# Performance work log

Hardware: AMD Instinct MI355X
Metric: run time of the kernel (lower is better)

## Reference

```python
import jax, jax.numpy as jnp
import numpy as np

NEGATIVE_RATIO = 3.0


def setup_inputs() -> dict:
    key = jax.random.key(0)
    k1, k2, k3, k4, k5 = jax.random.split(key, 5)
    B, N, C = 64, 8732, 81  # batch, num_priors (SSD300), num_classes (COCO)
    pred_conf = jax.random.normal(k1, (B, N, C), dtype=jnp.float32)
    pred_loc = jax.random.normal(k2, (B, N, 4), dtype=jnp.float32)
    labels = jax.random.randint(k3, (B, N), 1, C)
    is_pos = jax.random.uniform(k4, (B, N)) < 0.03
    labels = jnp.where(is_pos, labels, 0)
    labels = labels.at[:, 0].set(1)  # guarantee >=1 positive per image
    gt_conf = jax.nn.one_hot(labels, C, dtype=jnp.float32)
    pos = (labels > 0)[..., None].astype(jnp.float32)
    gt_loc = jax.random.normal(k5, (B, N, 4), dtype=jnp.float32) * pos
    return {"pred_conf": pred_conf, "pred_loc": pred_loc,
            "gt_conf": gt_conf, "gt_loc": gt_loc}


def reference(pred_conf, pred_loc, gt_conf, gt_loc):
    B, N, _ = pred_conf.shape
    # ----- conf loss: cross entropy against one-hot gt -----
    conf_loss = -(jax.nn.log_softmax(pred_conf, axis=-1) * gt_conf).sum(-1)  # [B, N]
    pos_mask = gt_conf[:, :, 0] == 0  # non-background priors
    num_pos = pos_mask.sum(-1).astype(pred_conf.dtype)  # [B]
    pos_conf_loss = jnp.where(pos_mask, conf_loss, 0.0).sum(-1)  # [B]
    # ----- hard negative mining: keep losses strictly above k-th largest negative loss -----
    num_neg = num_pos * NEGATIVE_RATIO  # [B], float
    neg_loss = jnp.where(pos_mask, 0.0, conf_loss)  # zero out positives
    sorted_desc = -jnp.sort(-neg_loss, axis=-1)  # descending per row
    k = jnp.clip(num_neg.astype(jnp.int32), 0, N - 1)  # [B]
    thresh = jnp.take_along_axis(sorted_desc, k[:, None], axis=-1)  # [B, 1]
    neg_mask = neg_loss > thresh  # only true on negatives (pos entries are 0)
    neg_conf_loss = jnp.where(neg_mask, conf_loss, 0.0).sum(-1)  # [B]
    conf_total = pos_conf_loss / num_pos + neg_conf_loss / num_neg  # [B]
    # ----- loc loss: smooth L1 on priors with nonzero gt_loc -----
    loc_mask = gt_loc != 0  # [B, N, 4]
    num_pos_loc = jnp.any(loc_mask, axis=-1).sum(-1).astype(pred_loc.dtype)  # [B]
    diff = jnp.abs(pred_loc - gt_loc)
    smooth_l1 = jnp.where(diff < 1.0, 0.5 * diff * diff, diff - 0.5)
    loc_total = jnp.where(loc_mask, smooth_l1, 0.0).sum((-1, -2)) / num_pos_loc  # [B]
    return (conf_total + loc_total).mean()
```

## Files before the change

### kernel.cpp

```cpp
#include <hip/hip_runtime.h>
#include <math.h>

#define BB 64
#define NN 8732
#define CC 81
#define ROWS 64
#define CBX ((NN + ROWS - 1) / ROWS)
#define LBX 5

__global__ void init_kernel(unsigned* acc, float* out) {
    int i = threadIdx.x;
    if (i < 4 * BB) acc[i] = 0u;
    if (i == 0) out[0] = 0.f;
}

__global__ __launch_bounds__(256) void fused_kernel(
        const float* __restrict__ pred_conf,
        const float* __restrict__ gt_conf,
        const float* __restrict__ pred_loc,
        const float* __restrict__ gt_loc,
        float* __restrict__ neg_loss,
        int* __restrict__ num_pos,
        float* __restrict__ pos_sum,
        float* __restrict__ loc_cnt,
        float* __restrict__ loc_sum) {
    const int b   = blockIdx.y;
    const int tid = threadIdx.x;

    if (blockIdx.x >= CBX) {
        const int lb = blockIdx.x - CBX;
        const float4* pl = (const float4*)pred_loc;
        const float4* gl = (const float4*)gt_loc;
        float sum = 0.f, cnt = 0.f;
        #pragma unroll
        for (int j = 0; j < 8; ++j) {
            int n = lb * 2048 + j * 256 + tid;
            if (n < NN) {
                size_t idx = (size_t)b * NN + n;
                float4 p = pl[idx];
                float4 g = gl[idx];
                bool any = false;
                float pv[4] = {p.x, p.y, p.z, p.w};
                float gv[4] = {g.x, g.y, g.z, g.w};
                #pragma unroll
                for (int c = 0; c < 4; ++c) {
                    if (gv[c] != 0.f) {
                        any = true;
                        float d = fabsf(pv[c] - gv[c]);
                        sum += (d < 1.f) ? 0.5f * d * d : d - 0.5f;
                    }
                }
                if (any) cnt += 1.f;
            }
        }
        for (int o = 32; o; o >>= 1) {
            sum += __shfl_down(sum, o, 64);
            cnt += __shfl_down(cnt, o, 64);
        }
        __shared__ float ls_sum, ls_cnt;
        if (tid == 0) { ls_sum = 0.f; ls_cnt = 0.f; }
        __syncthreads();
        if ((tid & 63) == 0) { atomicAdd(&ls_sum, sum); atomicAdd(&ls_cnt, cnt); }
        __syncthreads();
        if (tid == 0) { atomicAdd(&loc_sum[b], ls_sum); atomicAdd(&loc_cnt[b], ls_cnt); }
        return;
    }

    __shared__ float lbuf[ROWS * CC + 8];
    __shared__ int   s_cnt;
    __shared__ float s_sum;

    const int rowBase = blockIdx.x * ROWS;
    const int nrows   = min(ROWS, NN - rowBase);
    const size_t TOTF = (size_t)BB * NN * CC;

    if (tid == 0) { s_cnt = 0; s_sum = 0.f; }

    const size_t seg = ((size_t)b * NN + rowBase) * CC;
    const int    cnt = nrows * CC;
    const size_t a0  = seg & ~(size_t)3;
    const int  shift = (int)(seg - a0);
    const int   tot4 = (shift + cnt + 3) >> 2;

    const float4* g4 = (const float4*)(pred_conf + a0);
    float4*       l4 = (float4*)lbuf;
    for (int i = tid; i < tot4; i += 256) {
        size_t gf = a0 + 4 * (size_t)i;
        if (gf + 4 <= TOTF) {
            l4[i] = g4[i];
        } else {
            #pragma unroll
            for (int c = 0; c < 4; ++c)
                lbuf[4 * i + c] = (gf + c < TOTF) ? pred_conf[gf + c] : 0.f;
        }
    }
    __syncthreads();

    const int r = tid >> 2;
    const int h = tid & 3;
    if (r < nrows) {
        const int c0 = h * 20 + (h > 0 ? 1 : 0);
        const int nc = (h == 0) ? 21 : 20;
        const float* row = lbuf + shift + r * CC;
        const size_t gbase = ((size_t)b * NN + rowBase + r) * CC;
        const float gt0 = gt_conf[gbase];

        float v[21];
        #pragma unroll
        for (int j = 0; j < 21; ++j)
            v[j] = (j < nc) ? row[c0 + j] : -1e30f;

        float m = v[0];
        #pragma unroll
        for (int j = 1; j < 21; ++j) m = fmaxf(m, v[j]);
        m = fmaxf(m, __shfl_xor(m, 1, 64));
        m = fmaxf(m, __shfl_xor(m, 2, 64));

        float e = 0.f;
        #pragma unroll
        for (int j = 0; j < 21; ++j) e += __expf(v[j] - m);
        e += __shfl_xor(e, 1, 64);
        e += __shfl_xor(e, 2, 64);

        const bool pos = (gt0 == 0.f);
        float x_sel = v[0];
        if (pos) {
            float d = 0.f;
            #pragma unroll
            for (int j = 0; j < 21; ++j)
                if (j < nc) d += gt_conf[gbase + c0 + j] * v[j];
            d += __shfl_xor(d, 1, 64);
            d += __shfl_xor(d, 2, 64);
            x_sel = d;
        }

        const float loss = m + __logf(e) - x_sel;
        if (h == 0) {
            neg_loss[(size_t)b * NN + rowBase + r] = pos ? 0.f : loss;
            if (pos) { atomicAdd(&s_cnt, 1); atomicAdd(&s_sum, loss); }
        }
    }
    __syncthreads();
    if (tid == 0 && s_cnt) {
        atomicAdd(&num_pos[b], s_cnt);
        atomicAdd(&pos_sum[b], s_sum);
    }
}

__global__ __launch_bounds__(256) void select_kernel(
        const float* __restrict__ neg_loss,
        const int*   __restrict__ num_pos,
        const float* __restrict__ pos_sum,
        const float* __restrict__ loc_cnt,
        const float* __restrict__ loc_sum,
        float* __restrict__ out) {
    const int b    = blockIdx.x;
    const int tid  = threadIdx.x;
    const int lane = tid & 63;
    __shared__ unsigned vals[NN];
    __shared__ unsigned hist[256];
    __shared__ unsigned sh_prefix, sh_r;
    __shared__ float    s_part[4];

    #pragma unroll 4
    for (int i = tid; i < NN; i += 256)
        vals[i] = __float_as_uint(neg_loss[(size_t)b * NN + i]);

    const int np = num_pos[b];
    const int k  = min(3 * np, NN - 1);
    if (tid == 0) { sh_prefix = 0u; sh_r = (unsigned)k; }
    __syncthreads();

    unsigned prefix_mask = 0u;
    for (int p = 3; p >= 0; --p) {
        const unsigned pref = sh_prefix;
        const unsigned r    = sh_r;
        hist[tid] = 0u;
        __syncthreads();

        for (int i0 = 0; i0 < NN; i0 += 256) {
            const int i = i0 + tid;
            const bool act = (i < NN) && ((vals[i] & prefix_mask) == pref);
            const unsigned v   = act ? vals[i] : 0u;
            const unsigned bin = (v >> (8 * p)) & 255u;
            unsigned long long mm = __ballot(act);
            #pragma unroll
            for (int bit = 0; bit < 8; ++bit) {
                unsigned long long s = __ballot(act && ((bin >> bit) & 1u));
                mm &= ((bin >> bit) & 1u) ? s : ~s;
            }
            if (act && ((mm & ((1ull << lane) - 1ull)) == 0ull))
                atomicAdd(&hist[bin], (unsigned)__popcll(mm));
        }
        __syncthreads();

        if (tid < 64) {
            const unsigned h0 = hist[4 * tid + 0];
            const unsigned h1 = hist[4 * tid + 1];
            const unsigned h2 = hist[4 * tid + 2];
            const unsigned h3 = hist[4 * tid + 3];
            unsigned T = h0 + h1 + h2 + h3;
            #pragma unroll
            for (int off = 1; off < 64; off <<= 1) {
                unsigned t2 = __shfl_down(T, off, 64);
                if (tid + off < 64) T += t2;
            }
            unsigned Tn = __shfl_down(T, 1, 64);
            if (tid == 63) Tn = 0u;
            const unsigned S4 = Tn, S3 = S4 + h3, S2 = S3 + h2, S1 = S2 + h1, S0 = S1 + h0;
            int bin = -1; unsigned Slo = 0u;
            if      (S1 <= r && r < S0) { bin = 4 * tid + 0; Slo = S1; }
            else if (S2 <= r && r < S1) { bin = 4 * tid + 1; Slo = S2; }
            else if (S3 <= r && r < S2) { bin = 4 * tid + 2; Slo = S3; }
            else if (S4 <= r && r < S3) { bin = 4 * tid + 3; Slo = S4; }
            if (bin >= 0) {
                sh_r = r - Slo;
                sh_prefix = pref | ((unsigned)bin << (8 * p));
            }
        }
        __syncthreads();
        prefix_mask |= 0xFFu << (8 * p);
    }

    const float thresh = __uint_as_float(sh_prefix);
    float s = 0.f;
    #pragma unroll 4
    for (int i = tid; i < NN; i += 256) {
        float v = __uint_as_float(vals[i]);
        if (v > thresh) s += v;
    }
    for (int o = 32; o; o >>= 1) s += __shfl_down(s, o, 64);
    if (lane == 0) s_part[tid >> 6] = s;
    __syncthreads();
    if (tid == 0) {
        float neg_sum = s_part[0] + s_part[1] + s_part[2] + s_part[3];
        float npf = (float)np;
        float res = pos_sum[b] / npf + neg_sum / (3.0f * npf) + loc_sum[b] / loc_cnt[b];
        atomicAdd(out, res * (1.0f / BB));
    }
}

extern "C" void kernel_launch(void* const* d_in, const int* in_sizes, int n_in,
                              void* d_out, int out_size, void* d_ws, size_t ws_size,
                              hipStream_t stream) {
    const float* pred_conf = (const float*)d_in[0];
    const float* pred_loc  = (const float*)d_in[1];
    const float* gt_conf   = (const float*)d_in[2];
    const float* gt_loc    = (const float*)d_in[3];

    float* neg      = (float*)d_ws;
    int*   num_pos  = (int*)(neg + (size_t)BB * NN);
    float* pos_sum  = (float*)(num_pos + BB);
    float* loc_cnt  = pos_sum + BB;
    float* loc_sum  = loc_cnt + BB;

    init_kernel<<<1, 256, 0, stream>>>((unsigned*)num_pos, (float*)d_out);

    dim3 fgrid(CBX + LBX, BB);
    fused_kernel<<<fgrid, 256, 0, stream>>>(pred_conf, gt_conf, pred_loc, gt_loc,
                                            neg, num_pos, pos_sum, loc_cnt, loc_sum);

    select_kernel<<<BB, 256, 0, stream>>>(neg, num_pos, pos_sum, loc_cnt, loc_sum,
                                          (float*)d_out);
}
```

Before: 425.1 us.

## Register-prefetch next conf tile while computing current tile, four tiles per block

Each conf block now processes four 64-row tiles in sequence. While it computes the softmax for the current tile out of LDS, it holds the next tile's pred_conf in registers loaded as float4, so global loads overlap with compute. This cuts the block count by four and raises register use (24 extra floats per thread), which may lower occupancy and reduce how much the hardware can overlap across blocks.

```diff
diff --git a/kernel.cpp b/kernel.cpp
--- a/kernel.cpp
+++ b/kernel.cpp
@@ -4,14 +4,23 @@
 #define BB 64
 #define NN 8732
 #define CC 81
-#define ROWS 64
-#define CBX ((NN + ROWS - 1) / ROWS)
+#define TR 64
+#define TPB 4
+#define CBX ((NN + TR * TPB - 1) / (TR * TPB))
 #define LBX 5
 
 __global__ void init_kernel(unsigned* acc, float* out) {
     int i = threadIdx.x;
     if (i < 4 * BB) acc[i] = 0u;
     if (i == 0) out[0] = 0.f;
+}
+
+__device__ __forceinline__ float4 ld4g(const float* __restrict__ p, size_t gf, size_t TOTF) {
+    if (gf + 4 <= TOTF) return *(const float4*)(p + gf);
+    float4 r; float* rp = (float*)&r;
+    #pragma unroll
+    for (int c = 0; c < 4; ++c) rp[c] = (gf + c < TOTF) ? p[gf + c] : 0.f;
+    return r;
 }
 
 __global__ __launch_bounds__(256) void fused_kernel(
@@ -66,80 +75,107 @@
         return;
     }
 
-    __shared__ float lbuf[ROWS * CC + 8];
+    __shared__ float lbuf[TR * CC + 8];
     __shared__ int   s_cnt;
     __shared__ float s_sum;
-
-    const int rowBase = blockIdx.x * ROWS;
-    const int nrows   = min(ROWS, NN - rowBase);
+    float4* l4 = (float4*)lbuf;
+
     const size_t TOTF = (size_t)BB * NN * CC;
-
-    if (tid == 0) { s_cnt = 0; s_sum = 0.f; }
-
-    const size_t seg = ((size_t)b * NN + rowBase) * CC;
-    const int    cnt = nrows * CC;
-    const size_t a0  = seg & ~(size_t)3;
-    const int  shift = (int)(seg - a0);
-    const int   tot4 = (shift + cnt + 3) >> 2;
-
-    const float4* g4 = (const float4*)(pred_conf + a0);
-    float4*       l4 = (float4*)lbuf;
-    for (int i = tid; i < tot4; i += 256) {
-        size_t gf = a0 + 4 * (size_t)i;
-        if (gf + 4 <= TOTF) {
-            l4[i] = g4[i];
-        } else {
-            #pragma unroll
-            for (int c = 0; c < 4; ++c)
-                lbuf[4 * i + c] = (gf + c < TOTF) ? pred_conf[gf + c] : 0.f;
-        }
-    }
-    __syncthreads();
-
+    const int tile0 = blockIdx.x * TPB;
     const int r = tid >> 2;
     const int h = tid & 3;
-    if (r < nrows) {
-        const int c0 = h * 20 + (h > 0 ? 1 : 0);
-        const int nc = (h == 0) ? 21 : 20;
-        const float* row = lbuf + shift + r * CC;
-        const size_t gbase = ((size_t)b * NN + rowBase + r) * CC;
-        const float gt0 = gt_conf[gbase];
-
-        float v[21];
+
+    if (tid == 0) { s_cnt = 0; s_sum = 0.f; }
+
+    float4 rv[6];
+    float  gt0p;
+    int rowBn = tile0 * TR;
+    int nrn   = min(TR, NN - rowBn);
+    size_t a0n; int shn, t4n;
+    {
+        size_t seg = ((size_t)b * NN + rowBn) * CC;
+        a0n = seg & ~(size_t)3; shn = (int)(seg - a0n);
+        t4n = (shn + nrn * CC + 3) >> 2;
+    }
+    #pragma unroll
+    for (int j = 0; j < 6; ++j) {
+        int i = tid + 256 * j;
+        if (i < t4n) rv[j] = ld4g(pred_conf, a0n + 4 * (size_t)i, TOTF);
+    }
+    gt0p = (r < nrn) ? gt_conf[((size_t)b * NN + rowBn + r) * CC] : 1.f;
+
+    for (int t = 0; t < TPB; ++t) {
+        const int   c_rowB = rowBn, c_nr = nrn, c_sh = shn, c_t4 = t4n;
+        const float c_gt0  = gt0p;
+        if (c_rowB >= NN) break;
+
+        __syncthreads();
         #pragma unroll
-        for (int j = 0; j < 21; ++j)
-            v[j] = (j < nc) ? row[c0 + j] : -1e30f;
-
-        float m = v[0];
-        #pragma unroll
-        for (int j = 1; j < 21; ++j) m = fmaxf(m, v[j]);
-        m = fmaxf(m, __shfl_xor(m, 1, 64));
-        m = fmaxf(m, __shfl_xor(m, 2, 64));
-
-        float e = 0.f;
-        #pragma unroll
-        for (int j = 0; j < 21; ++j) e += __expf(v[j] - m);
-        e += __shfl_xor(e, 1, 64);
-        e += __shfl_xor(e, 2, 64);
-
-        const bool pos = (gt0 == 0.f);
-        float x_sel = v[0];
-        if (pos) {
-            float d = 0.f;
+        for (int j = 0; j < 6; ++j) {
+            int i = tid + 256 * j;
+            if (i < c_t4) l4[i] = rv[j];
+        }
+
+        const int nrowB = (tile0 + t + 1) * TR;
+        if (t + 1 < TPB && nrowB < NN) {
+            rowBn = nrowB; nrn = min(TR, NN - nrowB);
+            size_t seg = ((size_t)b * NN + nrowB) * CC;
+            a0n = seg & ~(size_t)3; shn = (int)(seg - a0n);
+            t4n = (shn + nrn * CC + 3) >> 2;
+            #pragma unroll
+            for (int j = 0; j < 6; ++j) {
+                int i = tid + 256 * j;
+                if (i < t4n) rv[j] = ld4g(pred_conf, a0n + 4 * (size_t)i, TOTF);
+            }
+            gt0p = (r < nrn) ? gt_conf[((size_t)b * NN + rowBn + r) * CC] : 1.f;
+        } else {
+            rowBn = NN;
+        }
+        __syncthreads();
+
+        if (r < c_nr) {
+            const int c0 = h * 20 + (h > 0 ? 1 : 0);
+            const int nc = (h == 0) ? 21 : 20;
+            const float* row = lbuf + c_sh + r * CC;
+            const size_t gbase = ((size_t)b * NN + c_rowB + r) * CC;
+
+            float v[21];
             #pragma unroll
             for (int j = 0; j < 21; ++j)
-                if (j < nc) d += gt_conf[gbase + c0 + j] * v[j];
-            d += __shfl_xor(d, 1, 64);
-            d += __shfl_xor(d, 2, 64);
-            x_sel = d;
-        }
-
-        const float loss = m + __logf(e) - x_sel;
-        if (h == 0) {
-            neg_loss[(size_t)b * NN + rowBase + r] = pos ? 0.f : loss;
-            if (pos) { atomicAdd(&s_cnt, 1); atomicAdd(&s_sum, loss); }
-        }
-    }
+                v[j] = (j < nc) ? row[c0 + j] : -1e30f;
+
+            float m = v[0];
+            #pragma unroll
+            for (int j = 1; j < 21; ++j) m = fmaxf(m, v[j]);
+            m = fmaxf(m, __shfl_xor(m, 1, 64));
+            m = fmaxf(m, __shfl_xor(m, 2, 64));
+
+            float e = 0.f;
+            #pragma unroll
+            for (int j = 0; j < 21; ++j) e += __expf(v[j] - m);
+            e += __shfl_xor(e, 1, 64);
+            e += __shfl_xor(e, 2, 64);
+
+            const bool pos = (c_gt0 == 0.f);
+            float x_sel = v[0];
+            if (pos) {
+                float d = 0.f;
+                #pragma unroll
+                for (int j = 0; j < 21; ++j)
+                    if (j < nc) d += gt_conf[gbase + c0 + j] * v[j];
+                d += __shfl_xor(d, 1, 64);
+                d += __shfl_xor(d, 2, 64);
+                x_sel = d;
+            }
+
+            const float loss = m + __logf(e) - x_sel;
+            if (h == 0) {
+                neg_loss[(size_t)b * NN + c_rowB + r] = pos ? 0.f : loss;
+                if (pos) { atomicAdd(&s_cnt, 1); atomicAdd(&s_sum, loss); }
+            }
+        }
+    }
+
     __syncthreads();
     if (tid == 0 && s_cnt) {
         atomicAdd(&num_pos[b], s_cnt);
```

After: 415.9 us. 1.02x faster.

## Replace LDS-staged conf tiles with wave-strip register pipeline, 16 lanes per row

Applied to the files above, without the earlier changes.

Drops the shared-memory staging of 64-row pred_conf tiles and the block-wide syncs. Each wave now walks a strip of 32 priors four rows at a time, with 16 lanes per row, and software-prefetches the next group's logits into registers while computing the current group. The loc-loss path now issues per-wave global atomics instead of a shared-memory pre-reduction. The intent is to remove LDS round trips and barriers and to hide load latency. In exchange, global loads become strided per lane (less coalesced than float4 staging) and there are more global atomics.

```diff
diff --git a/kernel.cpp b/kernel.cpp
--- a/kernel.cpp
+++ b/kernel.cpp
@@ -4,8 +4,10 @@
 #define BB 64
 #define NN 8732
 #define CC 81
-#define ROWS 64
-#define CBX ((NN + ROWS - 1) / ROWS)
+#define STRIP 32
+#define GPW 8
+#define CWAVES ((NN + STRIP - 1) / STRIP)
+#define CBX ((CWAVES + 3) / 4)
 #define LBX 5
 
 __global__ void init_kernel(unsigned* acc, float* out) {
@@ -57,93 +59,126 @@
             sum += __shfl_down(sum, o, 64);
             cnt += __shfl_down(cnt, o, 64);
         }
-        __shared__ float ls_sum, ls_cnt;
-        if (tid == 0) { ls_sum = 0.f; ls_cnt = 0.f; }
-        __syncthreads();
-        if ((tid & 63) == 0) { atomicAdd(&ls_sum, sum); atomicAdd(&ls_cnt, cnt); }
-        __syncthreads();
-        if (tid == 0) { atomicAdd(&loc_sum[b], ls_sum); atomicAdd(&loc_cnt[b], ls_cnt); }
+        if ((tid & 63) == 0) {
+            atomicAdd(&loc_sum[b], sum);
+            atomicAdd(&loc_cnt[b], cnt);
+        }
         return;
     }
 
-    __shared__ float lbuf[ROWS * CC + 8];
-    __shared__ int   s_cnt;
-    __shared__ float s_sum;
-
-    const int rowBase = blockIdx.x * ROWS;
-    const int nrows   = min(ROWS, NN - rowBase);
-    const size_t TOTF = (size_t)BB * NN * CC;
-
-    if (tid == 0) { s_cnt = 0; s_sum = 0.f; }
-
-    const size_t seg = ((size_t)b * NN + rowBase) * CC;
-    const int    cnt = nrows * CC;
-    const size_t a0  = seg & ~(size_t)3;
-    const int  shift = (int)(seg - a0);
-    const int   tot4 = (shift + cnt + 3) >> 2;
-
-    const float4* g4 = (const float4*)(pred_conf + a0);
-    float4*       l4 = (float4*)lbuf;
-    for (int i = tid; i < tot4; i += 256) {
-        size_t gf = a0 + 4 * (size_t)i;
-        if (gf + 4 <= TOTF) {
-            l4[i] = g4[i];
-        } else {
-            #pragma unroll
-            for (int c = 0; c < 4; ++c)
-                lbuf[4 * i + c] = (gf + c < TOTF) ? pred_conf[gf + c] : 0.f;
-        }
-    }
-    __syncthreads();
-
-    const int r = tid >> 2;
-    const int h = tid & 3;
-    if (r < nrows) {
-        const int c0 = h * 20 + (h > 0 ? 1 : 0);
-        const int nc = (h == 0) ? 21 : 20;
-        const float* row = lbuf + shift + r * CC;
-        const size_t gbase = ((size_t)b * NN + rowBase + r) * CC;
-        const float gt0 = gt_conf[gbase];
-
-        float v[21];
-        #pragma unroll
-        for (int j = 0; j < 21; ++j)
-            v[j] = (j < nc) ? row[c0 + j] : -1e30f;
-
-        float m = v[0];
-        #pragma unroll
-        for (int j = 1; j < 21; ++j) m = fmaxf(m, v[j]);
-        m = fmaxf(m, __shfl_xor(m, 1, 64));
-        m = fmaxf(m, __shfl_xor(m, 2, 64));
-
-        float e = 0.f;
-        #pragma unroll
-        for (int j = 0; j < 21; ++j) e += __expf(v[j] - m);
-        e += __shfl_xor(e, 1, 64);
-        e += __shfl_xor(e, 2, 64);
-
-        const bool pos = (gt0 == 0.f);
-        float x_sel = v[0];
-        if (pos) {
-            float d = 0.f;
-            #pragma unroll
-            for (int j = 0; j < 21; ++j)
-                if (j < nc) d += gt_conf[gbase + c0 + j] * v[j];
-            d += __shfl_xor(d, 1, 64);
-            d += __shfl_xor(d, 2, 64);
-            x_sel = d;
-        }
-
-        const float loss = m + __logf(e) - x_sel;
-        if (h == 0) {
-            neg_loss[(size_t)b * NN + rowBase + r] = pos ? 0.f : loss;
-            if (pos) { atomicAdd(&s_cnt, 1); atomicAdd(&s_sum, loss); }
-        }
-    }
-    __syncthreads();
-    if (tid == 0 && s_cnt) {
-        atomicAdd(&num_pos[b], s_cnt);
-        atomicAdd(&pos_sum[b], s_sum);
+    const int wave = tid >> 6;
+    const int lane = tid & 63;
+    const int sub  = lane & 15;
+    const int rw   = lane >> 4;
+
+    const int wid   = blockIdx.x * 4 + wave;
+    const int strip = wid * STRIP;
+    int ng = 0;
+    if (strip < NN) {
+        int nst = NN - strip; if (nst > STRIP) nst = STRIP;
+        ng = (nst + 3) >> 2;
+    }
+
+    int   my_cnt = 0;
+    float my_sum = 0.f;
+
+    float cv0, cv1, cv2, cv3, cv4, cv5, cg0;
+    int   c_n = 0; bool c_valid = false;
+
+    if (ng > 0) {
+        int n = strip + rw;
+        c_valid = (n < NN);
+        c_n = n;
+        int ncl = c_valid ? n : (NN - 1);
+        size_t base = ((size_t)b * NN + ncl) * CC;
+        cv0 = pred_conf[base + sub +  0];
+        cv1 = pred_conf[base + sub + 16];
+        cv2 = pred_conf[base + sub + 32];
+        cv3 = pred_conf[base + sub + 48];
+        cv4 = pred_conf[base + sub + 64];
+        cv5 = (sub == 0) ? pred_conf[base + 80] : -1e30f;
+        cg0 = gt_conf[base];
+    }
+
+    #pragma unroll
+    for (int gi = 0; gi < GPW; ++gi) {
+        if (gi >= ng) break;
+
+        float nv0, nv1, nv2, nv3, nv4, nv5, ngt0;
+        int   n_n = 0; bool n_valid = false;
+        if (gi + 1 < ng) {
+            int n = strip + (gi + 1) * 4 + rw;
+            n_valid = (n < NN);
+            n_n = n;
+            int ncl = n_valid ? n : (NN - 1);
+            size_t base = ((size_t)b * NN + ncl) * CC;
+            nv0 = pred_conf[base + sub +  0];
+            nv1 = pred_conf[base + sub + 16];
+            nv2 = pred_conf[base + sub + 32];
+            nv3 = pred_conf[base + sub + 48];
+            nv4 = pred_conf[base + sub + 64];
+            nv5 = (sub == 0) ? pred_conf[base + 80] : -1e30f;
+            ngt0 = gt_conf[base];
+        }
+
+        {
+            size_t base = ((size_t)b * NN + (c_valid ? c_n : (NN - 1))) * CC;
+
+            float m = fmaxf(fmaxf(fmaxf(cv0, cv1), fmaxf(cv2, cv3)), fmaxf(cv4, cv5));
+            m = fmaxf(m, __shfl_xor(m, 1, 64));
+            m = fmaxf(m, __shfl_xor(m, 2, 64));
+            m = fmaxf(m, __shfl_xor(m, 4, 64));
+            m = fmaxf(m, __shfl_xor(m, 8, 64));
+
+            const bool pos = (cg0 == 0.f);
+
+            float gv0 = 0.f, gv1 = 0.f, gv2 = 0.f, gv3 = 0.f, gv4 = 0.f, gv5 = 0.f;
+            if (pos) {
+                gv0 = gt_conf[base + sub +  0];
+                gv1 = gt_conf[base + sub + 16];
+                gv2 = gt_conf[base + sub + 32];
+                gv3 = gt_conf[base + sub + 48];
+                gv4 = gt_conf[base + sub + 64];
+                gv5 = (sub == 0) ? gt_conf[base + 80] : 0.f;
+            }
+
+            float e = __expf(cv0 - m) + __expf(cv1 - m) + __expf(cv2 - m)
+                    + __expf(cv3 - m) + __expf(cv4 - m);
+            e += (sub == 0) ? __expf(cv5 - m) : 0.f;
+            e += __shfl_xor(e, 1, 64);
+            e += __shfl_xor(e, 2, 64);
+            e += __shfl_xor(e, 4, 64);
+            e += __shfl_xor(e, 8, 64);
+
+            float x_sel = cv0;
+            if (pos) {
+                float d = cv0 * gv0 + cv1 * gv1 + cv2 * gv2 + cv3 * gv3 + cv4 * gv4;
+                d += (sub == 0) ? cv5 * gv5 : 0.f;
+                d += __shfl_xor(d, 1, 64);
+                d += __shfl_xor(d, 2, 64);
+                d += __shfl_xor(d, 4, 64);
+                d += __shfl_xor(d, 8, 64);
+                x_sel = d;
+            }
+
+            if (sub == 0 && c_valid) {
+                const float loss = m + __logf(e) - x_sel;
+                neg_loss[(size_t)b * NN + c_n] = pos ? 0.f : loss;
+                if (pos) { my_cnt++; my_sum += loss; }
+            }
+        }
+
+        cv0 = nv0; cv1 = nv1; cv2 = nv2; cv3 = nv3; cv4 = nv4; cv5 = nv5;
+        cg0 = ngt0; c_n = n_n; c_valid = n_valid;
+    }
+
+    my_sum += __shfl_down(my_sum, 32, 64);
+    my_cnt += __shfl_down(my_cnt, 32, 64);
+    my_sum += __shfl_down(my_sum, 16, 64);
+    my_cnt += __shfl_down(my_cnt, 16, 64);
+    if (lane == 0 && my_cnt) {
+        atomicAdd(&num_pos[b], my_cnt);
+        atomicAdd(&pos_sum[b], my_sum);
     }
 }
 
```

New measurement: 441.0 us. +3.7%, slower.
